# Kernel optimization log

Hardware: AMD Instinct MI355X
Metric: run time of the kernel (lower is better)

## Reference

```python
import jax, jax.numpy as jnp
import numpy as np

B, T, D, NH, C = 64, 256, 768, 12, 7
DH = D // NH

def setup_inputs() -> dict:
    key = jax.random.key(0)
    ks = jax.random.split(key, 8)
    s = 0.02
    H = jax.random.normal(ks[0], (B, T, D), jnp.float32)
    num_turns = jax.random.randint(ks[1], (B,), 1, T + 1)  # >=1 real turn each
    Wq = jax.random.normal(ks[2], (D, D), jnp.float32) * s
    Wk = jax.random.normal(ks[3], (D, D), jnp.float32) * s
    Wv = jax.random.normal(ks[4], (D, D), jnp.float32) * s
    Wo = jax.random.normal(ks[5], (D, D), jnp.float32) * s
    Wc = jax.random.normal(ks[6], (2 * D, C), jnp.float32) * s
    bq = jnp.zeros((D,), jnp.float32); bk = jnp.zeros((D,), jnp.float32)
    bv = jnp.zeros((D,), jnp.float32); bo = jnp.zeros((D,), jnp.float32)
    bc = jnp.zeros((C,), jnp.float32)
    return dict(H=H, Wq=Wq, bq=bq, Wk=Wk, bk=bk, Wv=Wv, bv=bv, Wo=Wo, bo=bo,
                Wc=Wc, bc=bc, num_turns=num_turns)

def reference(H, Wq, bq, Wk, bk, Wv, bv, Wo, bo, Wc, bc, num_turns):
    # Vectorized form of the per-(dialogue, turn) python loop:
    # turn t attends (multi-head) over strictly-earlier real turns.
    q = (H @ Wq + bq).reshape(B, T, NH, DH)
    k = (H @ Wk + bk).reshape(B, T, NH, DH)
    v = (H @ Wv + bv).reshape(B, T, NH, DH)
    scores = jnp.einsum('bqhd,bkhd->bhqk', q, k) / np.sqrt(DH).astype(np.float32)
    tq = jnp.arange(T)
    # strict causal (key < query) AND key is a real (non-padding) turn
    mask = (tq[None, :, None] > tq[None, None, :]) & (tq[None, None, :] < num_turns[:, None, None])  # [B,T,T]
    scores = jnp.where(mask[:, None], scores, -1e30)
    attn = jax.nn.softmax(scores, axis=-1)
    row_valid = mask.any(-1)  # [B,T]; False for t=0 (and beyond padding prefix logic)
    attn = jnp.where(row_valid[:, None, :, None], attn, 0.0)
    ctx = jnp.einsum('bhqk,bkhd->bqhd', attn, v).reshape(B, T, D)
    c = ctx @ Wo + bo
    # t==0: original sets c_t = exact zeros (no out-proj bias) -> zero full rows
    c = jnp.where(row_valid[:, :, None], c, 0.0)
    z = jnp.concatenate([H, c], axis=-1)          # [B,T,2D]
    all_logits = z @ Wc + bc                       # [B,T,C]
    final_logits = all_logits[jnp.arange(B), num_turns - 1]  # [B,C]
    return all_logits, final_logits
```

## Files before the change

### kernel.cpp

```cpp
#include <hip/hip_runtime.h>
#include <hip/hip_bf16.h>

#define B_  64
#define T_  256
#define D_  768
#define NH_ 12
#define DH_ 64
#define C_  7
#define QS_ 2304

using f32x4  = __attribute__((ext_vector_type(4))) float;
using bf16x8 = __attribute__((ext_vector_type(8))) __bf16;
using u16x8  = __attribute__((ext_vector_type(8))) unsigned short;
using u16x4  = __attribute__((ext_vector_type(4))) unsigned short;
using s16x4  = __attribute__((ext_vector_type(4))) short;

#if defined(__has_builtin)
#if __has_builtin(__builtin_amdgcn_mfma_f32_16x16x16bf16_1k)
#define HAS_MFMA16 1
#endif
#endif

static __device__ inline unsigned short f2bf(float f) {
    union { float f; unsigned u; } c; c.f = f;
    unsigned u = c.u;
    return (unsigned short)((u + 0x7fffu + ((u >> 16) & 1u)) >> 16);
}

#define ASYNC16(gp, lp) __builtin_amdgcn_global_load_lds(                      \
    (const __attribute__((address_space(1))) unsigned int*)(gp),               \
    (__attribute__((address_space(3))) unsigned int*)(lp), 16, 0, 0)

#define PRO_WF   13
#define PRO_BIAS 9
#define PRO_TR   1728
#define PRO_CONV 6144
#define PRO_ALL  (PRO_WF + PRO_BIAS + PRO_TR + PRO_CONV)

__global__ __launch_bounds__(256) void prologue(
    const float* __restrict__ H, unsigned short* __restrict__ Hb,
    const float* __restrict__ Wq, const float* __restrict__ Wk,
    const float* __restrict__ Wv,
    unsigned short* __restrict__ Wqkvt,
    const float* __restrict__ bq, const float* __restrict__ bk,
    const float* __restrict__ bv, float* __restrict__ bqkv,
    const float* __restrict__ Wo, const float* __restrict__ Wc,
    const float* __restrict__ bo,
    float* __restrict__ Wf, float* __restrict__ boc)
{
    __shared__ float tile[32][33];
    __shared__ float wcs[D_ * C_];
    const int blk = blockIdx.x;
    const int tid = threadIdx.x;

    if (blk < PRO_WF) {
        const int fb = blk;
        for (int i = tid; i < D_ * C_; i += 256)
            wcs[i] = Wc[(size_t)D_ * C_ + i];
        __syncthreads();
        if (fb < 12) {
            const int dl = tid >> 2;
            const int ks = tid & 3;
            const int d  = fb * 64 + dl;
            const float* wrow = Wo + (size_t)d * D_;
            float a[C_] = {};
            for (int e = ks * 192; e < ks * 192 + 192; ++e) {
                const float w = wrow[e];
#pragma unroll
                for (int c = 0; c < C_; ++c) a[c] += w * wcs[e * C_ + c];
            }
#pragma unroll
            for (int c = 0; c < C_; ++c) {
                a[c] += __shfl_xor(a[c], 1, 64);
                a[c] += __shfl_xor(a[c], 2, 64);
            }
            if (ks == 0) {
#pragma unroll
                for (int c = 0; c < C_; ++c) Wf[d * C_ + c] = a[c];
            }
        } else if (tid < C_) {
            float a = 0.f;
            for (int e = 0; e < D_; ++e) a += bo[e] * wcs[e * C_ + tid];
            boc[tid] = a;
        }
    } else if (blk < PRO_WF + PRO_BIAS) {
        const int i = (blk - PRO_WF) * 256 + tid;
        if (i < D_)          bqkv[i] = bq[i];
        else if (i < 2 * D_) bqkv[i] = bk[i - D_];
        else if (i < 3 * D_) bqkv[i] = bv[i - 2 * D_];
    } else if (blk < PRO_WF + PRO_BIAS + PRO_TR) {
        const int tb = blk - PRO_WF - PRO_BIAS;
        const int z = tb / 576;
        const int rem = tb - z * 576;
        const int bx = (rem % 24) * 32;
        const int by = (rem / 24) * 32;
        const size_t wsz = (size_t)D_ * D_;
        const float* W = (z == 0) ? Wq : (z == 1) ? Wk : Wv;
        unsigned short* Wt = Wqkvt + (size_t)z * wsz;
        const int tx = tid & 31;
        const int ty = tid >> 5;
#pragma unroll
        for (int i = ty; i < 32; i += 8)
            tile[i][tx] = W[(size_t)(by + i) * D_ + bx + tx];
        __syncthreads();
#pragma unroll
        for (int i = ty; i < 32; i += 8)
            Wt[(size_t)(bx + i) * D_ + by + tx] = f2bf(tile[tx][i]);
    } else {
        const int i = ((blk - PRO_WF - PRO_BIAS - PRO_TR) * 256 + tid) * 8;
        float4 f0 = *(const float4*)(H + i);
        float4 f1 = *(const float4*)(H + i + 4);
        u16x8 u;
        u[0] = f2bf(f0.x); u[1] = f2bf(f0.y); u[2] = f2bf(f0.z); u[3] = f2bf(f0.w);
        u[4] = f2bf(f1.x); u[5] = f2bf(f1.y); u[6] = f2bf(f1.z); u[7] = f2bf(f1.w);
        *(uint4*)(Hb + i) = __builtin_bit_cast(uint4, u);
    }
}

#define QBM 128
#define QBN 128
#define QBK 64
#define KQ  768
#define NKT 12

#define BAR   do { __builtin_amdgcn_s_barrier();                               \
                   __builtin_amdgcn_sched_barrier(0); } while (0)
#define VMW(n) do { asm volatile("s_waitcnt vmcnt(" #n ")" ::: "memory");      \
                    __builtin_amdgcn_sched_barrier(0); } while (0)

__global__ __launch_bounds__(512, 2) void gemm_qkv_db(
    const unsigned short* __restrict__ A,
    const unsigned short* __restrict__ Bt,
    const float* __restrict__ bias,
    unsigned short* __restrict__ qkvb,
    unsigned short* __restrict__ Vt,
    const int* __restrict__ num_turns)
{
    __shared__ unsigned short As[2][QBM * QBK];
    __shared__ unsigned short Bs[2][QBN * QBK];

    const int tid = threadIdx.x;
    const int wid = tid >> 6;
    const int ln  = tid & 63;
    const int hi  = ln >> 4;
    const int lo  = ln & 15;
    const int wm  = (wid & 3) * 32;
    const int wn  = (wid >> 2) * 64;

    const int L   = blockIdx.y * gridDim.x + blockIdx.x;
    const int wg  = (L & 7) * 288 + (L >> 3);
    const int my  = wg / 18;
    const int nx  = wg - my * 18;

    const int row0 = my * QBM;
    const int col0 = nx * QBN;

    if (col0 >= D_ && (row0 & (T_ - 1)) != 0) {
        if (num_turns[row0 >> 8] <= 128) return;
    }

    const int s0 = tid >> 3;
    const int ch = (tid & 7) ^ (s0 & 7);
    const unsigned short* a0 = A  + (size_t)(row0 + s0) * KQ + ch * 8;
    const unsigned short* b0 = Bt + (size_t)(col0 + s0) * KQ + ch * 8;

#define STG(t, q) do {                                                         \
    _Pragma("unroll") for (int c = 0; c < 2; ++c) {                            \
        ASYNC16(a0 + (size_t)(t) * QBK + (size_t)c * 64 * KQ,                  \
                &As[q][c * 4096 + wid * 512]);                                 \
        ASYNC16(b0 + (size_t)(t) * QBK + (size_t)c * 64 * KQ,                  \
                &Bs[q][c * 4096 + wid * 512]);                                 \
    }                                                                          \
} while (0)

    const int fcs[2] = { (0 * 4 + hi) ^ (lo & 7), (1 * 4 + hi) ^ (lo & 7) };

    f32x4 acc[2][4] = {};

#define TILE(t, q, qn) do {                                                    \
    if ((t) + 1 < NKT) { STG((t) + 1, qn); VMW(4); }                           \
    else               { VMW(0); }                                             \
    BAR;                                                                       \
    _Pragma("unroll") for (int s = 0; s < 2; ++s) {                            \
        const int fc = fcs[s];                                                 \
        bf16x8 af[2], bfr[4];                                                  \
        _Pragma("unroll") for (int i = 0; i < 2; ++i)                          \
            af[i] = *(const bf16x8*)&As[q][(wm + i * 16 + lo) * QBK + fc * 8]; \
        _Pragma("unroll") for (int j = 0; j < 4; ++j)                          \
            bfr[j] = *(const bf16x8*)&Bs[q][(wn + j * 16 + lo) * QBK + fc * 8];\
        __builtin_amdgcn_s_setprio(1);                                         \
        _Pragma("unroll") for (int i = 0; i < 2; ++i)                          \
        _Pragma("unroll") for (int j = 0; j < 4; ++j)                          \
            acc[i][j] = __builtin_amdgcn_mfma_f32_16x16x32_bf16(               \
                af[i], bfr[j], acc[i][j], 0, 0, 0);                            \
        __builtin_amdgcn_s_setprio(0);                                         \
    }                                                                          \
    BAR;                                                                       \
} while (0)

    STG(0, 0);
#pragma unroll
    for (int g = 0; g < NKT; g += 2) {
        TILE(g + 0, 0, 1);
        TILE(g + 1, 1, 0);
    }
#undef STG
#undef TILE

    const int bidx = row0 >> 8;
    const int t0   = row0 & (T_ - 1);
    if (col0 >= 1536) {
#pragma unroll
        for (int j = 0; j < 4; ++j) {
            const int dcol = (col0 - 1536) + wn + j * 16 + lo;
            const float bcol = bias[col0 + wn + j * 16 + lo];
            unsigned short* vrow =
                Vt + ((size_t)(bidx * NH_ + (dcol >> 6)) * DH_ + (dcol & 63)) * T_ + t0;
#pragma unroll
            for (int i = 0; i < 2; ++i) {
                u16x4 pk;
#pragma unroll
                for (int r = 0; r < 4; ++r) pk[r] = f2bf(acc[i][j][r] + bcol);
                *(u16x4*)(vrow + wm + i * 16 + hi * 4) = pk;
            }
        }
        return;
    }
#pragma unroll
    for (int j = 0; j < 4; ++j) {
        const int col = col0 + wn + j * 16 + lo;
        const float bcol = bias[col];
#pragma unroll
        for (int i = 0; i < 2; ++i) {
#pragma unroll
            for (int r = 0; r < 4; ++r) {
                const int row = row0 + wm + i * 16 + hi * 4 + r;
                qkvb[(size_t)row * QS_ + col] = f2bf(acc[i][j][r] + bcol);
            }
        }
    }
}

#if HAS_MFMA16
__global__ __launch_bounds__(512) void attn_fused(
    const unsigned short* __restrict__ qkv, const unsigned short* __restrict__ Vt,
    const int* __restrict__ num_turns, unsigned short* __restrict__ ctx)
{
    __shared__ unsigned short Klds[256 * 64];
    __shared__ unsigned short Vlds[64 * 256];

    const int bh = blockIdx.x;
    const int b = bh / NH_;
    const int h = bh - b * NH_;
    const int tid = threadIdx.x;
    const int wave = tid >> 6;
    const int lane = tid & 63;
    const int hi = lane >> 4;
    const int lo = lane & 15;
    const int lo7 = lo & 7;

    const int nt = num_turns[b];
    const int kend16 = (min(254, nt - 1) >> 4) + 1;
    const int vst = (kend16 <= 8) ? 128 : 256;

    const unsigned short* qb  = qkv + (size_t)(b * T_) * QS_ + h * DH_;
    const unsigned short* kb  = qb + D_;
    const unsigned short* vtb = Vt + (size_t)bh * DH_ * T_;

    {
        const int nr = kend16 * 2;
        for (int rd = wave; rd < nr; rd += 8) {
            const int row = rd * 8 + (lane >> 3);
            const int c   = (lane & 7) ^ (row & 7);
            ASYNC16(kb + (size_t)row * QS_ + c * 8, &Klds[rd * 512]);
        }
    }
    if (vst == 256) {
        for (int rd = wave; rd < 32; rd += 8) {
            const int d = rd * 2 + (lane >> 5);
            const int c = (lane & 31) ^ (d & 7);
            ASYNC16(vtb + (size_t)d * T_ + c * 8, &Vlds[rd * 512]);
        }
    } else {
        for (int rd = wave; rd < 16; rd += 8) {
            const int d = rd * 4 + (lane >> 4);
            const int c = (lane & 15) ^ (d & 7);
            ASYNC16(vtb + (size_t)d * T_ + c * 8, &Vlds[rd * 512]);
        }
    }

    bf16x8 aqs[2][2];
#pragma unroll
    for (int i = 0; i < 2; ++i) {
        const int m0 = (i ? (15 - wave) : wave) * 16;
#pragma unroll
        for (int ks = 0; ks < 2; ++ks)
            aqs[i][ks] = *(const bf16x8*)(qb + (size_t)(m0 + lo) * QS_ + ks * 32 + hi * 8);
    }

    asm volatile("s_waitcnt vmcnt(0)" ::: "memory");
    __syncthreads();

#pragma unroll
    for (int i = 0; i < 2; ++i) {
        const int tq = i ? (15 - wave) : wave;
        const int m0 = tq * 16;
        const int qrow = m0 + lo;
        const int kmax  = min(m0 + 14, nt - 1);
        const int ktmax = kmax >> 4;

        f32x4 s[16] = {};
#pragma unroll
        for (int kt = 0; kt < 16; ++kt) {
            if (kt <= ktmax) {
#pragma unroll
                for (int ks = 0; ks < 2; ++ks) {
                    bf16x8 kf = *(const bf16x8*)&Klds[(kt * 16 + lo) * 64
                                                     + ((ks * 4 + hi) ^ lo7) * 8];
                    s[kt] = __builtin_amdgcn_mfma_f32_16x16x32_bf16(kf, aqs[i][ks], s[kt], 0, 0, 0);
                }
            }
        }

        float lsum = 0.f;
        s16x4 pf[16];
#pragma unroll
        for (int kt = 0; kt < 16; ++kt) {
            if (kt <= ktmax) {
#pragma unroll
                for (int r = 0; r < 4; ++r) {
                    const int key = kt * 16 + hi * 4 + r;
                    const bool valid = (key < qrow) && (key < nt);
                    const float p = valid ? __expf(s[kt][r] * 0.125f) : 0.f;
                    lsum += p;
                    pf[kt][r] = (short)f2bf(p);
                }
            }
        }

        f32x4 o[4] = {};
#pragma unroll
        for (int kt = 0; kt < 16; ++kt) {
            if (kt <= ktmax) {
#pragma unroll
                for (int nd = 0; nd < 4; ++nd) {
                    const int cidx = (kt * 2 + (hi >> 1)) ^ lo7;
                    s16x4 bv = *(const s16x4*)&Vlds[(nd * 16 + lo) * vst
                                                    + cidx * 8 + (hi & 1) * 4];
                    o[nd] = __builtin_amdgcn_mfma_f32_16x16x16bf16_1k(pf[kt], bv, o[nd], 0, 0, 0);
                }
            }
        }

        lsum += __shfl_xor(lsum, 16, 64);
        lsum += __shfl_xor(lsum, 32, 64);
        float linv[4];
#pragma unroll
        for (int r = 0; r < 4; ++r) {
            const float lq = __shfl(lsum, hi * 4 + r, 64);
            linv[r] = (lq > 0.f) ? (1.f / lq) : 0.f;
        }

#pragma unroll
        for (int nd = 0; nd < 4; ++nd) {
#pragma unroll
            for (int r = 0; r < 4; ++r) {
                ctx[((size_t)(b * T_ + m0 + hi * 4 + r)) * D_ + h * DH_ + nd * 16 + lo]
                    = f2bf(o[nd][r] * linv[r]);
            }
        }
    }
}
#else
__global__ __launch_bounds__(512) void attn_fused(
    const unsigned short* __restrict__ qkv, const unsigned short* __restrict__ Vt,
    const int* __restrict__ num_turns, unsigned short* __restrict__ ctx)
{
    __shared__ unsigned short Plds[8][16 * 264];

    const int bh = blockIdx.x;
    const int b = bh / NH_;
    const int h = bh - b * NH_;
    const int tid = threadIdx.x;
    const int wave = tid >> 6;
    const int lane = tid & 63;
    const int hi = lane >> 4;
    const int lo = lane & 15;

    const int nt = num_turns[b];
    const unsigned short* qb = qkv + (size_t)(b * T_) * QS_ + h * DH_;
    const unsigned short* kb = qb + D_;
    const unsigned short* vtb = Vt + (size_t)bh * DH_ * T_;

    for (int ii = 0; ii < 2; ++ii) {
        const int m0 = (ii ? (15 - wave) : wave) * 16;
        const int kmax = min(m0 + 14, nt - 1);
        const int n0hi = (kmax >> 4) | 1;
        const int nks  = (kmax >> 5) + 1;

        bf16x8 aq[2];
#pragma unroll
        for (int ks = 0; ks < 2; ++ks)
            aq[ks] = *(const bf16x8*)(qb + (size_t)(m0 + lo) * QS_ + ks * 32 + hi * 8);

        f32x4 s[16] = {};
#pragma unroll
        for (int n0 = 0; n0 < 16; ++n0) {
            if (n0 <= n0hi) {
#pragma unroll
                for (int ks = 0; ks < 2; ++ks) {
                    bf16x8 bk = *(const bf16x8*)(kb + (size_t)(n0 * 16 + lo) * QS_ + ks * 32 + hi * 8);
                    s[n0] = __builtin_amdgcn_mfma_f32_16x16x32_bf16(aq[ks], bk, s[n0], 0, 0, 0);
                }
            }
        }

#pragma unroll
        for (int r = 0; r < 4; ++r) {
            const int qrow = m0 + hi * 4 + r;
            float mr = -1e30f;
#pragma unroll
            for (int n0 = 0; n0 < 16; ++n0) {
                if (n0 <= n0hi) {
                    int key = n0 * 16 + lo;
                    bool valid = (key < qrow) && (key < nt);
                    float se = valid ? s[n0][r] * 0.125f : -1e30f;
                    s[n0][r] = se;
                    mr = fmaxf(mr, se);
                }
            }
#pragma unroll
            for (int off = 1; off < 16; off <<= 1) mr = fmaxf(mr, __shfl_xor(mr, off, 64));

            float lr = 0.f;
#pragma unroll
            for (int n0 = 0; n0 < 16; ++n0) {
                if (n0 <= n0hi) {
                    float se = s[n0][r];
                    float pv = (se > -5e29f) ? __expf(se - mr) : 0.f;
                    s[n0][r] = pv;
                    lr += pv;
                }
            }
#pragma unroll
            for (int off = 1; off < 16; off <<= 1) lr += __shfl_xor(lr, off, 64);

            float inv = (lr > 0.f) ? (1.f / lr) : 0.f;
#pragma unroll
            for (int n0 = 0; n0 < 16; ++n0) {
                if (n0 <= n0hi) {
                    Plds[wave][(hi * 4 + r) * 264 + n0 * 16 + lo] = f2bf(s[n0][r] * inv);
                }
            }
        }

        f32x4 o[4] = {};
#pragma unroll
        for (int ks = 0; ks < 8; ++ks) {
            if (ks < nks) {
                const unsigned short* lp = &Plds[wave][lo * 264 + ks * 32 + hi * 8];
                bf16x8 ap = __builtin_bit_cast(bf16x8, *(const uint4*)lp);
#pragma unroll
                for (int nd = 0; nd < 4; ++nd) {
                    bf16x8 bvf = *(const bf16x8*)(vtb + (size_t)(nd * 16 + lo) * T_ + ks * 32 + hi * 8);
                    o[nd] = __builtin_amdgcn_mfma_f32_16x16x32_bf16(ap, bvf, o[nd], 0, 0, 0);
                }
            }
        }

#pragma unroll
        for (int nd = 0; nd < 4; ++nd) {
#pragma unroll
            for (int r = 0; r < 4; ++r) {
                ctx[((size_t)(b * T_ + m0 + hi * 4 + r)) * D_ + h * DH_ + nd * 16 + lo]
                    = f2bf(o[nd][r]);
            }
        }
    }
}
#endif

#define WCP 1544

__global__ __launch_bounds__(256) void logits_mfma(
    const unsigned short* __restrict__ Hb, const unsigned short* __restrict__ ctxb,
    const float* __restrict__ Wc, const float* __restrict__ Wf,
    const float* __restrict__ bc, const float* __restrict__ boc,
    const int* __restrict__ num_turns, float* __restrict__ out)
{
    __shared__ unsigned short sW[16 * WCP];

    const int tid = threadIdx.x;
    const int wave = tid >> 6;
    const int lane = tid & 63;
    const int hi = lane >> 4;
    const int lo = lane & 15;

    for (int i = tid; i < 16 * 1536; i += 256) {
        int n = i & 15, kk = i >> 4;
        float val = 0.f;
        if (n < C_)
            val = (kk < D_) ? Wc[(size_t)kk * C_ + n] : Wf[(kk - D_) * C_ + n];
        sW[n * WCP + kk] = f2bf(val);
    }
    __syncthreads();

    const int m0 = blockIdx.x * 64 + wave * 16;
    const unsigned short* hrow = Hb   + (size_t)(m0 + lo) * D_;
    const unsigned short* crow = ctxb + (size_t)(m0 + lo) * D_;

    f32x4 acc = {};
#pragma unroll
    for (int kt = 0; kt < 24; ++kt) {
        bf16x8 a = *(const bf16x8*)(hrow + kt * 32 + hi * 8);
        bf16x8 w = *(const bf16x8*)&sW[lo * WCP + kt * 32 + hi * 8];
        acc = __builtin_amdgcn_mfma_f32_16x16x32_bf16(a, w, acc, 0, 0, 0);
    }
#pragma unroll
    for (int kt = 0; kt < 24; ++kt) {
        bf16x8 a = *(const bf16x8*)(crow + kt * 32 + hi * 8);
        bf16x8 w = *(const bf16x8*)&sW[lo * WCP + (768 + kt * 32) + hi * 8];
        acc = __builtin_amdgcn_mfma_f32_16x16x32_bf16(a, w, acc, 0, 0, 0);
    }

    if (lo < C_) {
        const float b0 = bc[lo];
        const float b1 = boc[lo];
#pragma unroll
        for (int r = 0; r < 4; ++r) {
            const int row = m0 + hi * 4 + r;
            const int t = row & (T_ - 1);
            const float tot = acc[r] + b0 + ((t != 0) ? b1 : 0.f);
            out[(size_t)row * C_ + lo] = tot;
            const int b = row >> 8;
            if (t == num_turns[b] - 1)
                out[(size_t)B_ * T_ * C_ + (size_t)b * C_ + lo] = tot;
        }
    }
}

extern "C" void kernel_launch(void* const* d_in, const int* in_sizes, int n_in,
                              void* d_out, int out_size, void* d_ws, size_t ws_size,
                              hipStream_t stream)
{
    const float* H  = (const float*)d_in[0];
    const float* Wq = (const float*)d_in[1];
    const float* bq = (const float*)d_in[2];
    const float* Wk = (const float*)d_in[3];
    const float* bk = (const float*)d_in[4];
    const float* Wv = (const float*)d_in[5];
    const float* bv = (const float*)d_in[6];
    const float* Wo = (const float*)d_in[7];
    const float* bo = (const float*)d_in[8];
    const float* Wc = (const float*)d_in[9];
    const float* bc = (const float*)d_in[10];
    const int* num_turns = (const int*)d_in[11];
    float* out = (float*)d_out;

    const int M = B_ * T_;
    const size_t per = (size_t)M * D_;
    const size_t wsz = (size_t)D_ * D_;

    unsigned short* ws16 = (unsigned short*)d_ws;
    unsigned short* Hb    = ws16;
    unsigned short* Wqkvt = Hb + per;
    unsigned short* qkvb  = Wqkvt + 3 * wsz;
    unsigned short* ctxb  = qkvb + (size_t)M * QS_;
    unsigned short* Vtb   = ctxb + per;
    float* bqkv = (float*)(Vtb + per);
    float* Wf   = bqkv + QS_;
    float* boc  = Wf + (size_t)D_ * C_;

    prologue<<<PRO_ALL, 256, 0, stream>>>(H, Hb, Wq, Wk, Wv, Wqkvt,
                                          bq, bk, bv, bqkv,
                                          Wo, Wc, bo, Wf, boc);

    dim3 qkvGrid(18, 128);
    gemm_qkv_db<<<qkvGrid, 512, 0, stream>>>(Hb, Wqkvt, bqkv, qkvb,
                                             Vtb, num_turns);

    attn_fused<<<B_ * NH_, 512, 0, stream>>>(qkvb, Vtb, num_turns, ctxb);

    logits_mfma<<<M / 64, 256, 0, stream>>>(Hb, ctxb, Wc, Wf, bc, boc,
                                            num_turns, out);
}
```

Before: 253.5 us.

## Enlarge QKV GEMM tiles to 256x256 with eight-phase interleaved load/MFMA pipeline

The QKV projection GEMM moves from 128x128 to 256x256 block tiles. Each wave now computes a 128x64 sub-tile with 8x4 accumulators, and each K-step is split into four phases that interleave LDS fragment reads, async global-to-LDS staging of half-tiles and MFMA groups between barriers. The per-block early exit for padded K/V rows is replaced by idling the upper-half waves whose rows are padding. The goal is more data reuse per byte loaded and better overlap of memory with compute. The costs are more register pressure, a possible loss of occupancy, fewer blocks on the grid, and barrier-heavy phases in which dead waves still take part.

New measurement: 263.7 us. 1.04x slower.

```diff
diff --git a/kernel.cpp b/kernel.cpp
--- a/kernel.cpp
+++ b/kernel.cpp
@@ -117,18 +117,20 @@
     }
 }
 
-#define QBM 128
-#define QBN 128
+#define QBM 256
+#define QBN 256
 #define QBK 64
 #define KQ  768
 #define NKT 12
 
 #define BAR   do { __builtin_amdgcn_s_barrier();                               \
                    __builtin_amdgcn_sched_barrier(0); } while (0)
+#define LGKM0 do { asm volatile("s_waitcnt lgkmcnt(0)" ::: "memory");          \
+                   __builtin_amdgcn_sched_barrier(0); } while (0)
 #define VMW(n) do { asm volatile("s_waitcnt vmcnt(" #n ")" ::: "memory");      \
                     __builtin_amdgcn_sched_barrier(0); } while (0)
 
-__global__ __launch_bounds__(512, 2) void gemm_qkv_db(
+__global__ __launch_bounds__(512, 2) void gemm_qkv_8ph(
     const unsigned short* __restrict__ A,
     const unsigned short* __restrict__ Bt,
     const float* __restrict__ bias,
@@ -144,80 +146,119 @@
     const int ln  = tid & 63;
     const int hi  = ln >> 4;
     const int lo  = ln & 15;
-    const int wm  = (wid & 3) * 32;
-    const int wn  = (wid >> 2) * 64;
-
-    const int L   = blockIdx.y * gridDim.x + blockIdx.x;
-    const int wg  = (L & 7) * 288 + (L >> 3);
-    const int my  = wg / 18;
-    const int nx  = wg - my * 18;
-
+    const int wm  = (wid >> 2) * 128;
+    const int wn  = (wid & 3) * 64;
+
+    const int L  = blockIdx.y * gridDim.x + blockIdx.x;
+    const int wg = (L & 7) * 72 + (L >> 3);
+    const int my = wg / 9;
+    const int nx = wg - my * 9;
     const int row0 = my * QBM;
     const int col0 = nx * QBN;
 
-    if (col0 >= D_ && (row0 & (T_ - 1)) != 0) {
-        if (num_turns[row0 >> 8] <= 128) return;
-    }
+    const int  ntb      = num_turns[my];
+    const bool deadwave = (col0 >= D_) && (wm == 128) && (ntb <= 128);
 
     const int s0 = tid >> 3;
     const int ch = (tid & 7) ^ (s0 & 7);
     const unsigned short* a0 = A  + (size_t)(row0 + s0) * KQ + ch * 8;
     const unsigned short* b0 = Bt + (size_t)(col0 + s0) * KQ + ch * 8;
 
-#define STG(t, q) do {                                                         \
-    _Pragma("unroll") for (int c = 0; c < 2; ++c) {                            \
-        ASYNC16(a0 + (size_t)(t) * QBK + (size_t)c * 64 * KQ,                  \
-                &As[q][c * 4096 + wid * 512]);                                 \
-        ASYNC16(b0 + (size_t)(t) * QBK + (size_t)c * 64 * KQ,                  \
-                &Bs[q][c * 4096 + wid * 512]);                                 \
-    }                                                                          \
+#define STG_AH(t, q, h) do {                                                   \
+    ASYNC16(a0 + (size_t)(t) * QBK + (size_t)((h) * 64) * KQ,                  \
+            &As[q][(h) * 4096 + wid * 512]);                                   \
+    ASYNC16(a0 + (size_t)(t) * QBK + (size_t)((h) * 64 + 128) * KQ,            \
+            &As[q][(h) * 4096 + 8192 + wid * 512]);                            \
 } while (0)
+#define STG_BH(t, q, h) do {                                                   \
+    ASYNC16(b0 + (size_t)(t) * QBK + (size_t)((h) * 128) * KQ,                 \
+            &Bs[q][(h) * 8192 + wid * 512]);                                   \
+    ASYNC16(b0 + (size_t)(t) * QBK + (size_t)((h) * 128 + 64) * KQ,            \
+            &Bs[q][(h) * 8192 + 4096 + wid * 512]);                            \
+} while (0)
 
     const int fcs[2] = { (0 * 4 + hi) ^ (lo & 7), (1 * 4 + hi) ^ (lo & 7) };
 
-    f32x4 acc[2][4] = {};
-
-#define TILE(t, q, qn) do {                                                    \
-    if ((t) + 1 < NKT) { STG((t) + 1, qn); VMW(4); }                           \
-    else               { VMW(0); }                                             \
+    f32x4  acc[8][4] = {};
+    bf16x8 af[4][2];
+    bf16x8 bf0[2][2];
+    bf16x8 bf1[2][2];
+
+#define RD_A(q, half) do {                                                     \
+  _Pragma("unroll") for (int mf = 0; mf < 4; ++mf)                             \
+  _Pragma("unroll") for (int ks = 0; ks < 2; ++ks)                             \
+    af[mf][ks] = *(const bf16x8*)&As[q][(wm + (half) * 64 + mf * 16 + lo) * QBK + fcs[ks] * 8]; \
+} while (0)
+#define RD_B(q, dst, off) do {                                                 \
+  _Pragma("unroll") for (int nf = 0; nf < 2; ++nf)                             \
+  _Pragma("unroll") for (int ks = 0; ks < 2; ++ks)                             \
+    dst[nf][ks] = *(const bf16x8*)&Bs[q][(wn + (off) + nf * 16 + lo) * QBK + fcs[ks] * 8]; \
+} while (0)
+#define MM(i0, j0, bsrc) do {                                                  \
+  __builtin_amdgcn_s_setprio(1);                                               \
+  _Pragma("unroll") for (int mf = 0; mf < 4; ++mf)                             \
+  _Pragma("unroll") for (int nf = 0; nf < 2; ++nf)                             \
+  _Pragma("unroll") for (int ks = 0; ks < 2; ++ks)                             \
+    acc[(i0) + mf][(j0) + nf] = __builtin_amdgcn_mfma_f32_16x16x32_bf16(       \
+        af[mf][ks], bsrc[nf][ks], acc[(i0) + mf][(j0) + nf], 0, 0, 0);         \
+  __builtin_amdgcn_s_setprio(0);                                               \
+} while (0)
+
+#define GROUP(gg, q_, qn_) do {                                                \
+                                                             \
+    if (!deadwave) { RD_A(q_, 0); RD_B(q_, bf0, 0); }                          \
+    if ((gg) + 1 < NKT) STG_AH((gg) + 1, qn_, 1);                              \
+    BAR; LGKM0;                                                                \
+    if (!deadwave) MM(0, 0, bf0);                                              \
     BAR;                                                                       \
-    _Pragma("unroll") for (int s = 0; s < 2; ++s) {                            \
-        const int fc = fcs[s];                                                 \
-        bf16x8 af[2], bfr[4];                                                  \
-        _Pragma("unroll") for (int i = 0; i < 2; ++i)                          \
-            af[i] = *(const bf16x8*)&As[q][(wm + i * 16 + lo) * QBK + fc * 8]; \
-        _Pragma("unroll") for (int j = 0; j < 4; ++j)                          \
-            bfr[j] = *(const bf16x8*)&Bs[q][(wn + j * 16 + lo) * QBK + fc * 8];\
-        __builtin_amdgcn_s_setprio(1);                                         \
-        _Pragma("unroll") for (int i = 0; i < 2; ++i)                          \
-        _Pragma("unroll") for (int j = 0; j < 4; ++j)                          \
-            acc[i][j] = __builtin_amdgcn_mfma_f32_16x16x32_bf16(               \
-                af[i], bfr[j], acc[i][j], 0, 0, 0);                            \
-        __builtin_amdgcn_s_setprio(0);                                         \
-    }                                                                          \
+                                                             \
+    if (!deadwave) RD_B(q_, bf1, 32);                                          \
+    if ((gg) + 2 < NKT) STG_AH((gg) + 2, q_, 0);                               \
+    BAR; LGKM0;                                                                \
+    if (!deadwave) MM(0, 2, bf1);                                              \
+    BAR;                                                                       \
+                                                             \
+    if (!deadwave) RD_A(q_, 1);                                                \
+    if ((gg) + 2 < NKT) STG_BH((gg) + 2, q_, 0);                               \
+    BAR; LGKM0;                                                                \
+    if (!deadwave) MM(4, 2, bf1);                                              \
+    BAR;                                                                       \
+                                              \
+    if ((gg) + 2 < NKT) { STG_BH((gg) + 2, q_, 1); VMW(6); }                   \
+    else if ((gg) + 1 < NKT) VMW(0);                                           \
+    BAR; LGKM0;                                                                \
+    if (!deadwave) MM(4, 0, bf0);                                              \
     BAR;                                                                       \
 } while (0)
 
-    STG(0, 0);
+    STG_AH(0, 0, 0); STG_BH(0, 0, 0); STG_BH(0, 0, 1); STG_AH(0, 0, 1);
+    STG_AH(1, 1, 0); STG_BH(1, 1, 0); STG_BH(1, 1, 1);
+    VMW(6); BAR;
+
 #pragma unroll
     for (int g = 0; g < NKT; g += 2) {
-        TILE(g + 0, 0, 1);
-        TILE(g + 1, 1, 0);
-    }
-#undef STG
-#undef TILE
-
-    const int bidx = row0 >> 8;
-    const int t0   = row0 & (T_ - 1);
+        GROUP(g + 0, 0, 1);
+        GROUP(g + 1, 1, 0);
+    }
+#undef STG_AH
+#undef STG_BH
+#undef RD_A
+#undef RD_B
+#undef MM
+#undef GROUP
+
+    if (deadwave) return;
+
+    const int t0 = row0 & (T_ - 1);
     if (col0 >= 1536) {
 #pragma unroll
         for (int j = 0; j < 4; ++j) {
             const int dcol = (col0 - 1536) + wn + j * 16 + lo;
             const float bcol = bias[col0 + wn + j * 16 + lo];
             unsigned short* vrow =
-                Vt + ((size_t)(bidx * NH_ + (dcol >> 6)) * DH_ + (dcol & 63)) * T_ + t0;
-#pragma unroll
-            for (int i = 0; i < 2; ++i) {
+                Vt + ((size_t)(my * NH_ + (dcol >> 6)) * DH_ + (dcol & 63)) * T_ + t0;
+#pragma unroll
+            for (int i = 0; i < 8; ++i) {
                 u16x4 pk;
 #pragma unroll
                 for (int r = 0; r < 4; ++r) pk[r] = f2bf(acc[i][j][r] + bcol);
@@ -231,7 +272,7 @@
         const int col = col0 + wn + j * 16 + lo;
         const float bcol = bias[col];
 #pragma unroll
-        for (int i = 0; i < 2; ++i) {
+        for (int i = 0; i < 8; ++i) {
 #pragma unroll
             for (int r = 0; r < 4; ++r) {
                 const int row = row0 + wm + i * 16 + hi * 4 + r;
@@ -575,9 +616,9 @@
                                           bq, bk, bv, bqkv,
                                           Wo, Wc, bo, Wf, boc);
 
-    dim3 qkvGrid(18, 128);
-    gemm_qkv_db<<<qkvGrid, 512, 0, stream>>>(Hb, Wqkvt, bqkv, qkvb,
-                                             Vtb, num_turns);
+    dim3 qkvGrid(9, 64);
+    gemm_qkv_8ph<<<qkvGrid, 512, 0, stream>>>(Hb, Wqkvt, bqkv, qkvb,
+                                              Vtb, num_turns);
 
     attn_fused<<<B_ * NH_, 512, 0, stream>>>(qkvb, Vtb, num_turns, ctxb);
 
```
